# Performance work log

Hardware: AMD Instinct MI355X
Metric: run time of the kernel (lower is better)

The kernel has to match this reference:

```python
import jax, jax.numpy as jnp
import numpy as np

B, S, D, H = 1, 2048, 1024, 16
HD = D // H
FF = 4 * D
EPS_LN = 1e-5
EPS_ATTN = 1e-6


def _layernorm(x, g, b):
    mu = jnp.mean(x, axis=-1, keepdims=True)
    var = jnp.mean(jnp.square(x - mu), axis=-1, keepdims=True)
    return (x - mu) * jax.lax.rsqrt(var + EPS_LN) * g + b


def setup_inputs() -> dict:
    key = jax.random.key(0)
    ks = jax.random.split(key, 12)
    w = lambda k, shape: (jax.random.normal(k, shape, jnp.float32) * 0.02)
    return {
        "x": jax.random.normal(ks[0], (B, S, D), jnp.float32),
        "Wq": w(ks[1], (D, D)), "bq": jnp.zeros((D,), jnp.float32),
        "Wk": w(ks[2], (D, D)), "bk": jnp.zeros((D,), jnp.float32),
        "Wv": w(ks[3], (D, D)), "bv": jnp.zeros((D,), jnp.float32),
        "Wo": w(ks[4], (D, D)), "bo": jnp.zeros((D,), jnp.float32),
        "W1": w(ks[5], (FF, D)), "bb1": jnp.zeros((FF,), jnp.float32),
        "W2": w(ks[6], (D, FF)), "bb2": jnp.zeros((D,), jnp.float32),
        "g1": jnp.ones((D,), jnp.float32), "be1": jnp.zeros((D,), jnp.float32),
        "g2": jnp.ones((D,), jnp.float32), "be2": jnp.zeros((D,), jnp.float32),
    }


def reference(x, Wq, bq, Wk, bk, Wv, bv, Wo, bo, W1, bb1, W2, bb2, g1, be1, g2, be2):
    # --- pre-norm causal linear attention ---
    h = _layernorm(x, g1, be1)                     # (B,S,D)
    def heads(t):
        return t.reshape(B, S, H, HD).transpose(0, 2, 1, 3)  # (B,H,S,hd)
    q = heads(h @ Wq.T + bq)
    k = heads(h @ Wk.T + bk)
    v = heads(h @ Wv.T + bv)
    # feature map phi(x) = elu(x) + 1 (strictly positive)
    q = jax.nn.elu(q) + 1.0
    k = jax.nn.elu(k) + 1.0
    # causal cumulative state: S_t = sum_{i<=t} k_i v_i^T ; z_t = sum_{i<=t} k_i
    kv = jnp.cumsum(jnp.einsum("bhsd,bhse->bhsde", k, v), axis=2)  # (B,H,S,hd,hd)
    z = jnp.cumsum(k, axis=2)                                       # (B,H,S,hd)
    num = jnp.einsum("bhsd,bhsde->bhse", q, kv)                    # (B,H,S,hd)
    den = jnp.einsum("bhsd,bhsd->bhs", q, z) + EPS_ATTN
    attn = (num / den[..., None]).transpose(0, 2, 1, 3).reshape(B, S, D)
    attn = attn @ Wo.T + bo
    x = x + attn
    # --- FFN (GELU exact, matching torch nn.GELU default) ---
    h2 = _layernorm(x, g2, be2)
    ff = jax.nn.gelu(h2 @ W1.T + bb1, approximate=False) @ W2.T + bb2
    return x + ff
```

## Files before the change

### kernel.cpp

```cpp
#include <hip/hip_runtime.h>
#include <hip/hip_bf16.h>
#include <math.h>

constexpr int S  = 2048;
constexpr int D  = 1024;
constexpr int H  = 16;
constexpr int HD = 64;
constexpr int FF = 4096;
constexpr int NC  = 32;
constexpr int CHK = 64;
constexpr int QS  = 3 * D;

typedef __attribute__((ext_vector_type(8))) short bf16x8;
typedef __attribute__((ext_vector_type(4))) float f32x4;

__device__ inline unsigned short f2bf(float f) {
    unsigned int u = __float_as_uint(f);
    u = (u + 0x7FFFu + ((u >> 16) & 1u)) >> 16;
    return (unsigned short)u;
}

constexpr int DD4 = D * D / 4;
constexpr int FD4 = FF * D / 4;
constexpr int CVT_TOTAL4 = 4 * DD4 + 2 * FD4;
constexpr int NB_CVT  = CVT_TOTAL4 / 256;

__global__ __launch_bounds__(256) void prep(const float* __restrict__ Wq,
                                            const float* __restrict__ Wk,
                                            const float* __restrict__ Wv,
                                            const float* __restrict__ Wo,
                                            const float* __restrict__ W1,
                                            const float* __restrict__ W2,
                                            unsigned short* __restrict__ Wqkvb,
                                            unsigned short* __restrict__ Wob,
                                            unsigned short* __restrict__ W1b,
                                            unsigned short* __restrict__ W2b,
                                            const float* __restrict__ x,
                                            const float* __restrict__ g1,
                                            const float* __restrict__ be1,
                                            unsigned short* __restrict__ h1) {
    const int b = blockIdx.x, tid = threadIdx.x;
    if (b < NB_CVT) {
        int i = b * 256 + tid;
        const float* s;
        unsigned short* dp;
        if (i < DD4)                 { s = Wq + (size_t)i * 4;               dp = Wqkvb + (size_t)i * 4; }
        else if (i < 2 * DD4)        { s = Wk + (size_t)(i - DD4) * 4;       dp = Wqkvb + (size_t)i * 4; }
        else if (i < 3 * DD4)        { s = Wv + (size_t)(i - 2 * DD4) * 4;   dp = Wqkvb + (size_t)i * 4; }
        else if (i < 4 * DD4)        { s = Wo + (size_t)(i - 3 * DD4) * 4;   dp = Wob + (size_t)(i - 3 * DD4) * 4; }
        else if (i < 4 * DD4 + FD4)  { s = W1 + (size_t)(i - 4 * DD4) * 4;   dp = W1b + (size_t)(i - 4 * DD4) * 4; }
        else                         { s = W2 + (size_t)(i - 4 * DD4 - FD4) * 4; dp = W2b + (size_t)(i - 4 * DD4 - FD4) * 4; }
        float4 v = *(const float4*)s;
        ushort4 o = { f2bf(v.x), f2bf(v.y), f2bf(v.z), f2bf(v.w) };
        *(ushort4*)dp = o;
    } else {
        const int row = b - NB_CVT;
        float4 v = ((const float4*)(x + (size_t)row * D))[tid];
        float s  = v.x + v.y + v.z + v.w;
        float ss = v.x*v.x + v.y*v.y + v.z*v.z + v.w*v.w;
        #pragma unroll
        for (int off = 32; off > 0; off >>= 1) {
            s  += __shfl_down(s, off);
            ss += __shfl_down(ss, off);
        }
        __shared__ float sw[4], ssw[4];
        if ((tid & 63) == 0) { sw[tid >> 6] = s; ssw[tid >> 6] = ss; }
        __syncthreads();
        s  = sw[0] + sw[1] + sw[2] + sw[3];
        ss = ssw[0] + ssw[1] + ssw[2] + ssw[3];
        const float mu = s * (1.0f / D);
        const float rs = rsqrtf(ss * (1.0f / D) - mu * mu + 1e-5f);
        float4 gv = ((const float4*)g1)[tid];
        float4 bv = ((const float4*)be1)[tid];
        ushort4 o = { f2bf((v.x - mu) * rs * gv.x + bv.x),
                      f2bf((v.y - mu) * rs * gv.y + bv.y),
                      f2bf((v.z - mu) * rs * gv.z + bv.z),
                      f2bf((v.w - mu) * rs * gv.w + bv.w) };
        ((ushort4*)(h1 + (size_t)row * D))[tid] = o;
    }
}

template <int KS>
__global__ __launch_bounds__(256) void reduce_ln(const float* __restrict__ part,
                                                 const float* __restrict__ bias,
                                                 const float* __restrict__ res,
                                                 float* __restrict__ x2,
                                                 const float* __restrict__ g,
                                                 const float* __restrict__ b,
                                                 unsigned short* __restrict__ out) {
    const int row = blockIdx.x, tid = threadIdx.x;
    const size_t i4 = (size_t)row * 256 + tid;
    float4 a = ((const float4*)part)[i4];
    #pragma unroll
    for (int z = 1; z < KS; ++z) {
        float4 p = ((const float4*)part)[(size_t)z * S * 256 + i4];
        a.x += p.x; a.y += p.y; a.z += p.z; a.w += p.w;
    }
    float4 bi = ((const float4*)bias)[tid];
    float4 r  = ((const float4*)res)[i4];
    a.x += bi.x + r.x; a.y += bi.y + r.y; a.z += bi.z + r.z; a.w += bi.w + r.w;
    ((float4*)x2)[i4] = a;
    float s  = a.x + a.y + a.z + a.w;
    float ss = a.x*a.x + a.y*a.y + a.z*a.z + a.w*a.w;
    #pragma unroll
    for (int off = 32; off > 0; off >>= 1) {
        s  += __shfl_down(s, off);
        ss += __shfl_down(ss, off);
    }
    __shared__ float sw[4], ssw[4];
    if ((tid & 63) == 0) { sw[tid >> 6] = s; ssw[tid >> 6] = ss; }
    __syncthreads();
    s  = sw[0] + sw[1] + sw[2] + sw[3];
    ss = ssw[0] + ssw[1] + ssw[2] + ssw[3];
    const float mu = s * (1.0f / D);
    const float rs = rsqrtf(ss * (1.0f / D) - mu * mu + 1e-5f);
    float4 gv = ((const float4*)g)[tid];
    float4 bv = ((const float4*)b)[tid];
    ushort4 o = { f2bf((a.x - mu) * rs * gv.x + bv.x),
                  f2bf((a.y - mu) * rs * gv.y + bv.y),
                  f2bf((a.z - mu) * rs * gv.z + bv.z),
                  f2bf((a.w - mu) * rs * gv.w + bv.w) };
    ((ushort4*)(out + (size_t)row * D))[tid] = o;
}

template <int KS>
__global__ __launch_bounds__(256) void reduce_bias_res(const float* __restrict__ part,
                                                       const float* __restrict__ bias,
                                                       const float* __restrict__ res,
                                                       float* __restrict__ out,
                                                       int N4, int total4) {
    int i = blockIdx.x * 256 + threadIdx.x;
    if (i >= total4) return;
    float4 a = ((const float4*)part)[i];
    #pragma unroll
    for (int z = 1; z < KS; ++z) {
        float4 p = ((const float4*)part)[(size_t)z * total4 + i];
        a.x += p.x; a.y += p.y; a.z += p.z; a.w += p.w;
    }
    float4 b = ((const float4*)bias)[i % N4];
    float4 r = ((const float4*)res)[i];
    a.x += b.x + r.x; a.y += b.y + r.y; a.z += b.z + r.z; a.w += b.w + r.w;
    ((float4*)out)[i] = a;
}

enum { EPI_F32 = 0, EPI_QKV = 1, EPI_GELU_BF16 = 2, EPI_PART = 3 };

template <int EPI>
__global__ __launch_bounds__(256, 3) void gemm_bt(const unsigned short* __restrict__ A,
                                                  const unsigned short* __restrict__ W,
                                                  const float* __restrict__ bias,
                                                  const float* __restrict__ bias2,
                                                  const float* __restrict__ bias3,
                                                  void* __restrict__ outp,
                                                  int M, int N, int K, int kSplit) {
    __shared__ unsigned short As[2][64 * 64];
    __shared__ unsigned short Bs[2][128 * 64];
    const int tid  = threadIdx.x;
    const int tileM = blockIdx.x * 64;
    const int tileN = blockIdx.y * 128;
    const int w    = tid >> 6, lane = tid & 63;
    const int wm   = (w >> 1) * 32, wn = (w & 1) * 64;
    const int lr   = lane & 15, lk = lane >> 4;
    const int sw   = (lr >> 1) & 7;
    const int kLen   = K / kSplit;
    const int kStart = blockIdx.z * kLen;
    const int kEnd   = kStart + kLen;

    f32x4 acc[2][4];
    #pragma unroll
    for (int i = 0; i < 2; ++i)
        #pragma unroll
        for (int j = 0; j < 4; ++j) acc[i][j] = (f32x4)(0.0f);

    auto stage = [&](int buf, int k0) {
        #pragma unroll
        for (int p = 0; p < 2; ++p) {
            const int c   = p * 256 + tid;
            const int row = c >> 3;
            const int kc  = (c & 7) ^ ((row >> 1) & 7);
            __builtin_amdgcn_global_load_lds(
                (const __attribute__((address_space(1))) unsigned int*)
                    (A + (size_t)(tileM + row) * K + k0 + kc * 8),
                (__attribute__((address_space(3))) unsigned int*)&As[buf][c * 8],
                16, 0, 0);
        }
        #pragma unroll
        for (int p = 0; p < 4; ++p) {
            const int c   = p * 256 + tid;
            const int row = c >> 3;
            const int kc  = (c & 7) ^ ((row >> 1) & 7);
            __builtin_amdgcn_global_load_lds(
                (const __attribute__((address_space(1))) unsigned int*)
                    (W + (size_t)(tileN + row) * K + k0 + kc * 8),
                (__attribute__((address_space(3))) unsigned int*)&Bs[buf][c * 8],
                16, 0, 0);
        }
    };

    stage(0, kStart);
    __syncthreads();
    int buf = 0;
    for (int k0 = kStart; k0 < kEnd; k0 += 64) {
        if (k0 + 64 < kEnd) stage(buf ^ 1, k0 + 64);
        #pragma unroll
        for (int kk = 0; kk < 2; ++kk) {
            bf16x8 af[2], bfv[4];
            #pragma unroll
            for (int i = 0; i < 2; ++i) {
                const int row = wm + i * 16 + lr;
                af[i] = *(const bf16x8*)&As[buf][row * 64 + ((((kk << 2) | lk) ^ sw) << 3)];
            }
            #pragma unroll
            for (int j = 0; j < 4; ++j) {
                const int row = wn + j * 16 + lr;
                bfv[j] = *(const bf16x8*)&Bs[buf][row * 64 + ((((kk << 2) | lk) ^ sw) << 3)];
            }
            #pragma unroll
            for (int i = 0; i < 2; ++i)
                #pragma unroll
                for (int j = 0; j < 4; ++j)
                    acc[i][j] = __builtin_amdgcn_mfma_f32_16x16x32_bf16(af[i], bfv[j], acc[i][j], 0, 0, 0);
        }
        __syncthreads();
        buf ^= 1;
    }

    #pragma unroll
    for (int i = 0; i < 2; ++i) {
        const int rbase = tileM + wm + i * 16 + lk * 4;
        #pragma unroll
        for (int j = 0; j < 4; ++j) {
            const int col = tileN + wn + j * 16 + lr;
            #pragma unroll
            for (int r = 0; r < 4; ++r) {
                const int row = rbase + r;
                const size_t off = (size_t)row * N + col;
                float v = acc[i][j][r];
                if constexpr (EPI == EPI_PART) {
                    ((float*)outp)[(size_t)blockIdx.z * (size_t)M * (size_t)N + off] = v;
                } else if constexpr (EPI == EPI_QKV) {
                    float bc = (col < D) ? bias[col] : ((col < 2 * D) ? bias2[col - D] : bias3[col - 2 * D]);
                    v += bc;
                    if (col < 2 * D) v = v > 0.0f ? v + 1.0f : __expf(v);
                    ((float*)outp)[off] = v;
                } else if constexpr (EPI == EPI_GELU_BF16) {
                    v += bias[col];
                    float gl = 0.5f * v * (1.0f + erff(v * 0.70710678118654752f));
                    ((unsigned short*)outp)[off] = f2bf(gl);
                } else {
                    v += bias[col];
                    ((float*)outp)[off] = v;
                }
            }
        }
    }
}

__global__ __launch_bounds__(256) void attn_chunk_sums(const float* __restrict__ qkv,
                                                       float* __restrict__ KVc,
                                                       float* __restrict__ Zc) {
    const int c = blockIdx.x, h = blockIdx.y, tid = threadIdx.x;
    __shared__ float Kc[CHK * HD], Vc[CHK * HD];
    const int s0 = c * CHK;
    #pragma unroll
    for (int p = 0; p < 4; ++p) {
        int cc = p * 256 + tid;
        int t = cc >> 4, dp = (cc & 15) * 4;
        *(float4*)&Kc[t * HD + dp] = *(const float4*)(qkv + (size_t)(s0 + t) * QS + D     + h * HD + dp);
        *(float4*)&Vc[t * HD + dp] = *(const float4*)(qkv + (size_t)(s0 + t) * QS + 2 * D + h * HD + dp);
    }
    __syncthreads();
    const int d = tid >> 2, e0 = (tid & 3) * 16;
    float acc[16];
    #pragma unroll
    for (int j = 0; j < 16; ++j) acc[j] = 0.0f;
    float zacc = 0.0f;
    for (int t = 0; t < CHK; ++t) {
        float kv = Kc[t * HD + d];
        zacc += kv;
        #pragma unroll
        for (int j = 0; j < 16; ++j) acc[j] += kv * Vc[t * HD + e0 + j];
    }
    float* op = KVc + ((size_t)(h * NC + c) * HD + d) * HD + e0;
    #pragma unroll
    for (int j = 0; j < 16; ++j) op[j] = acc[j];
    if ((tid & 3) == 0) Zc[(size_t)(h * NC + c) * HD + d] = zacc;
}

__global__ __launch_bounds__(256) void attn_prefix(float* __restrict__ KVc,
                                                   float* __restrict__ Zc) {
    const int h = blockIdx.y;
    const int elem = blockIdx.x * 256 + threadIdx.x;
    size_t base = (size_t)h * NC * (HD * HD) + elem;
    float run = 0.0f;
    for (int c = 0; c < NC; ++c) {
        float t = KVc[base + (size_t)c * (HD * HD)];
        KVc[base + (size_t)c * (HD * HD)] = run;
        run += t;
    }
    if (blockIdx.x == 0 && threadIdx.x < HD) {
        size_t zb = (size_t)h * NC * HD + threadIdx.x;
        float zr = 0.0f;
        for (int c = 0; c < NC; ++c) {
            float t = Zc[zb + (size_t)c * HD];
            Zc[zb + (size_t)c * HD] = zr;
            zr += t;
        }
    }
}

__global__ __launch_bounds__(256) void attn_out(const float* __restrict__ qkv,
                                                const float* __restrict__ KVpre,
                                                const float* __restrict__ Zpre,
                                                unsigned short* __restrict__ attn) {
    const int c = blockIdx.x, h = blockIdx.y, tid = threadIdx.x;
    __shared__ float Qc[CHK * HD], KVs[CHK * HD], Pre[HD * HD], Sc[CHK * CHK];
    __shared__ float zp[HD], den[CHK];
    const int s0 = c * CHK;
    #pragma unroll
    for (int p = 0; p < 4; ++p) {
        int cc = p * 256 + tid;
        int t = cc >> 4, dp = (cc & 15) * 4;
        *(float4*)&Qc[t * HD + dp]  = *(const float4*)(qkv + (size_t)(s0 + t) * QS +     h * HD + dp);
        *(float4*)&KVs[t * HD + dp] = *(const float4*)(qkv + (size_t)(s0 + t) * QS + D + h * HD + dp);
        ((float4*)Pre)[cc] = *(const float4*)(KVpre + (size_t)(h * NC + c) * (HD * HD) + cc * 4);
    }
    if (tid < HD) zp[tid] = Zpre[(size_t)(h * NC + c) * HD + tid];
    __syncthreads();

    const int tt = tid >> 2, i0 = (tid & 3) * 16;
    for (int i = i0; i < i0 + 16; ++i) {
        float sv = 0.0f;
        for (int d2 = 0; d2 < HD; ++d2) sv += Qc[tt * HD + d2] * KVs[i * HD + d2];
        Sc[tt * CHK + i] = (i <= tt) ? sv : 0.0f;
    }
    __syncthreads();

    if (tid < CHK) {
        float dv = 1e-6f;
        for (int d2 = 0; d2 < HD; ++d2) dv += Qc[tid * HD + d2] * zp[d2];
        for (int i = 0; i < CHK; ++i) dv += Sc[tid * CHK + i];
        den[tid] = dv;
    }
    #pragma unroll
    for (int p = 0; p < 4; ++p) {
        int cc = p * 256 + tid;
        int t = cc >> 4, dp = (cc & 15) * 4;
        *(float4*)&KVs[t * HD + dp] = *(const float4*)(qkv + (size_t)(s0 + t) * QS + 2 * D + h * HD + dp);
    }
    __syncthreads();

    float o[16];
    #pragma unroll
    for (int j = 0; j < 16; ++j) o[j] = 0.0f;
    for (int d2 = 0; d2 < HD; ++d2) {
        float qv = Qc[tt * HD + d2];
        float sv = Sc[tt * CHK + d2];
        #pragma unroll
        for (int j = 0; j < 16; ++j)
            o[j] += qv * Pre[d2 * HD + i0 + j] + sv * KVs[d2 * HD + i0 + j];
    }
    const float inv = 1.0f / den[tt];
    unsigned short* op = attn + (size_t)(s0 + tt) * D + h * HD + i0;
    #pragma unroll
    for (int j0 = 0; j0 < 16; j0 += 4) {
        ushort4 ov = { f2bf(o[j0] * inv), f2bf(o[j0 + 1] * inv),
                       f2bf(o[j0 + 2] * inv), f2bf(o[j0 + 3] * inv) };
        *(ushort4*)(op + j0) = ov;
    }
}

extern "C" void kernel_launch(void* const* d_in, const int* in_sizes, int n_in,
                              void* d_out, int out_size, void* d_ws, size_t ws_size,
                              hipStream_t stream) {
    const float* x   = (const float*)d_in[0];
    const float* Wq  = (const float*)d_in[1];
    const float* bq  = (const float*)d_in[2];
    const float* Wk  = (const float*)d_in[3];
    const float* bk  = (const float*)d_in[4];
    const float* Wv  = (const float*)d_in[5];
    const float* bv  = (const float*)d_in[6];
    const float* Wo  = (const float*)d_in[7];
    const float* bo  = (const float*)d_in[8];
    const float* W1  = (const float*)d_in[9];
    const float* b1  = (const float*)d_in[10];
    const float* W2  = (const float*)d_in[11];
    const float* b2  = (const float*)d_in[12];
    const float* g1  = (const float*)d_in[13];
    const float* be1 = (const float*)d_in[14];
    const float* g2  = (const float*)d_in[15];
    const float* be2 = (const float*)d_in[16];
    float* out = (float*)d_out;

    char* wsp = (char*)d_ws;
    auto alloc = [&](size_t bytes) {
        char* p = wsp;
        wsp += (bytes + 255) & ~(size_t)255;
        return p;
    };
    unsigned short* h1   = (unsigned short*)alloc((size_t)S * D * 2);
    unsigned short* attn = (unsigned short*)alloc((size_t)S * D * 2);
    unsigned short* gbuf = (unsigned short*)alloc((size_t)S * FF * 2);
    float* x2   = (float*)alloc((size_t)S * D * 4);
    unsigned short* Wqkvb = (unsigned short*)alloc((size_t)3 * D * D * 2);
    unsigned short* Wob   = (unsigned short*)alloc((size_t)D * D * 2);
    unsigned short* W1b   = (unsigned short*)alloc((size_t)FF * D * 2);
    unsigned short* W2b   = (unsigned short*)alloc((size_t)D * FF * 2);
    float* KVc  = (float*)alloc((size_t)H * NC * HD * HD * 4);
    float* Zc   = (float*)alloc((size_t)H * NC * HD * 4);
    char* uni = (char*)alloc((size_t)32 * 1024 * 1024);
    float* qkv   = (float*)uni;
    float* parts = (float*)uni;

    prep<<<NB_CVT + S, 256, 0, stream>>>(Wq, Wk, Wv, Wo, W1, W2,
                                         Wqkvb, Wob, W1b, W2b,
                                         x, g1, be1, h1);

    gemm_bt<EPI_QKV><<<dim3(S / 64, 3 * D / 128, 1), 256, 0, stream>>>(
        h1, Wqkvb, bq, bk, bv, qkv, S, 3 * D, D, 1);

    attn_chunk_sums<<<dim3(NC, H), 256, 0, stream>>>(qkv, KVc, Zc);
    attn_prefix<<<dim3(16, H), 256, 0, stream>>>(KVc, Zc);
    attn_out<<<dim3(NC, H), 256, 0, stream>>>(qkv, KVc, Zc, attn);

    gemm_bt<EPI_PART><<<dim3(S / 64, D / 128, 2), 256, 0, stream>>>(
        attn, Wob, nullptr, nullptr, nullptr, parts, S, D, D, 2);
    reduce_ln<2><<<S, 256, 0, stream>>>(parts, bo, x, x2, g2, be2, h1);

    gemm_bt<EPI_GELU_BF16><<<dim3(S / 64, FF / 128, 1), 256, 0, stream>>>(
        h1, W1b, b1, nullptr, nullptr, gbuf, S, FF, D, 1);

    gemm_bt<EPI_PART><<<dim3(S / 64, D / 128, 4), 256, 0, stream>>>(
        gbuf, W2b, nullptr, nullptr, nullptr, parts, S, D, FF, 4);
    reduce_bias_res<4><<<(S * D / 4 + 255) / 256, 256, 0, stream>>>(
        parts, b2, x2, out, D / 4, S * D / 4);
}
```

Baseline: 288.6 us.

## Replace LDS-staged GEMM with register-direct 128x128 tiles loading fragments from global

The GEMM drops its shared-memory double buffering. Each wave now loads its MFMA fragments straight from global memory into registers, with a two-stage register prefetch. The block tile grows from 64x128 to 128x128, so each wave holds a 4x4 grid of accumulators, and the Wo projection split-K goes from 2 to 4 to keep enough blocks in flight. This removes LDS traffic and barriers. In exchange there is no sharing of operands across waves, so global and L2 traffic per FLOP is higher and register pressure rises, which may lower occupancy.

```diff
diff --git a/kernel.cpp b/kernel.cpp
--- a/kernel.cpp
+++ b/kernel.cpp
@@ -153,80 +153,60 @@
                                                   const float* __restrict__ bias3,
                                                   void* __restrict__ outp,
                                                   int M, int N, int K, int kSplit) {
-    __shared__ unsigned short As[2][64 * 64];
-    __shared__ unsigned short Bs[2][128 * 64];
     const int tid  = threadIdx.x;
-    const int tileM = blockIdx.x * 64;
+    const int tileM = blockIdx.x * 128;
     const int tileN = blockIdx.y * 128;
     const int w    = tid >> 6, lane = tid & 63;
-    const int wm   = (w >> 1) * 32, wn = (w & 1) * 64;
+    const int wm   = (w >> 1) * 64, wn = (w & 1) * 64;
     const int lr   = lane & 15, lk = lane >> 4;
-    const int sw   = (lr >> 1) & 7;
     const int kLen   = K / kSplit;
     const int kStart = blockIdx.z * kLen;
     const int kEnd   = kStart + kLen;
 
-    f32x4 acc[2][4];
-    #pragma unroll
-    for (int i = 0; i < 2; ++i)
+    const unsigned short* pA = A + (size_t)(tileM + wm + lr) * K + lk * 8;
+    const unsigned short* pB = W + (size_t)(tileN + wn + lr) * K + lk * 8;
+    const size_t rsA = (size_t)16 * K;
+
+    f32x4 acc[4][4];
+    #pragma unroll
+    for (int i = 0; i < 4; ++i)
         #pragma unroll
         for (int j = 0; j < 4; ++j) acc[i][j] = (f32x4)(0.0f);
 
-    auto stage = [&](int buf, int k0) {
-        #pragma unroll
-        for (int p = 0; p < 2; ++p) {
-            const int c   = p * 256 + tid;
-            const int row = c >> 3;
-            const int kc  = (c & 7) ^ ((row >> 1) & 7);
-            __builtin_amdgcn_global_load_lds(
-                (const __attribute__((address_space(1))) unsigned int*)
-                    (A + (size_t)(tileM + row) * K + k0 + kc * 8),
-                (__attribute__((address_space(3))) unsigned int*)&As[buf][c * 8],
-                16, 0, 0);
+    bf16x8 a0[4], b0[4], a1[4], b1[4];
+    #pragma unroll
+    for (int i = 0; i < 4; ++i) {
+        a0[i] = *(const bf16x8*)(pA + i * rsA + kStart);
+        b0[i] = *(const bf16x8*)(pB + i * rsA + kStart);
+    }
+
+    for (int k0 = kStart; k0 < kEnd; k0 += 64) {
+        #pragma unroll
+        for (int i = 0; i < 4; ++i) {
+            a1[i] = *(const bf16x8*)(pA + i * rsA + k0 + 32);
+            b1[i] = *(const bf16x8*)(pB + i * rsA + k0 + 32);
         }
         #pragma unroll
-        for (int p = 0; p < 4; ++p) {
-            const int c   = p * 256 + tid;
-            const int row = c >> 3;
-            const int kc  = (c & 7) ^ ((row >> 1) & 7);
-            __builtin_amdgcn_global_load_lds(
-                (const __attribute__((address_space(1))) unsigned int*)
-                    (W + (size_t)(tileN + row) * K + k0 + kc * 8),
-                (__attribute__((address_space(3))) unsigned int*)&Bs[buf][c * 8],
-                16, 0, 0);
+        for (int i = 0; i < 4; ++i)
+            #pragma unroll
+            for (int j = 0; j < 4; ++j)
+                acc[i][j] = __builtin_amdgcn_mfma_f32_16x16x32_bf16(a0[i], b0[j], acc[i][j], 0, 0, 0);
+        if (k0 + 64 < kEnd) {
+            #pragma unroll
+            for (int i = 0; i < 4; ++i) {
+                a0[i] = *(const bf16x8*)(pA + i * rsA + k0 + 64);
+                b0[i] = *(const bf16x8*)(pB + i * rsA + k0 + 64);
+            }
         }
-    };
-
-    stage(0, kStart);
-    __syncthreads();
-    int buf = 0;
-    for (int k0 = kStart; k0 < kEnd; k0 += 64) {
-        if (k0 + 64 < kEnd) stage(buf ^ 1, k0 + 64);
-        #pragma unroll
-        for (int kk = 0; kk < 2; ++kk) {
-            bf16x8 af[2], bfv[4];
+        #pragma unroll
+        for (int i = 0; i < 4; ++i)
             #pragma unroll
-            for (int i = 0; i < 2; ++i) {
-                const int row = wm + i * 16 + lr;
-                af[i] = *(const bf16x8*)&As[buf][row * 64 + ((((kk << 2) | lk) ^ sw) << 3)];
-            }
-            #pragma unroll
-            for (int j = 0; j < 4; ++j) {
-                const int row = wn + j * 16 + lr;
-                bfv[j] = *(const bf16x8*)&Bs[buf][row * 64 + ((((kk << 2) | lk) ^ sw) << 3)];
-            }
-            #pragma unroll
-            for (int i = 0; i < 2; ++i)
-                #pragma unroll
-                for (int j = 0; j < 4; ++j)
-                    acc[i][j] = __builtin_amdgcn_mfma_f32_16x16x32_bf16(af[i], bfv[j], acc[i][j], 0, 0, 0);
-        }
-        __syncthreads();
-        buf ^= 1;
-    }
-
-    #pragma unroll
-    for (int i = 0; i < 2; ++i) {
+            for (int j = 0; j < 4; ++j)
+                acc[i][j] = __builtin_amdgcn_mfma_f32_16x16x32_bf16(a1[i], b1[j], acc[i][j], 0, 0, 0);
+    }
+
+    #pragma unroll
+    for (int i = 0; i < 4; ++i) {
         const int rbase = tileM + wm + i * 16 + lk * 4;
         #pragma unroll
         for (int j = 0; j < 4; ++j) {
@@ -416,21 +396,21 @@
                                          Wqkvb, Wob, W1b, W2b,
                                          x, g1, be1, h1);
 
-    gemm_bt<EPI_QKV><<<dim3(S / 64, 3 * D / 128, 1), 256, 0, stream>>>(
+    gemm_bt<EPI_QKV><<<dim3(S / 128, 3 * D / 128, 1), 256, 0, stream>>>(
         h1, Wqkvb, bq, bk, bv, qkv, S, 3 * D, D, 1);
 
     attn_chunk_sums<<<dim3(NC, H), 256, 0, stream>>>(qkv, KVc, Zc);
     attn_prefix<<<dim3(16, H), 256, 0, stream>>>(KVc, Zc);
     attn_out<<<dim3(NC, H), 256, 0, stream>>>(qkv, KVc, Zc, attn);
 
-    gemm_bt<EPI_PART><<<dim3(S / 64, D / 128, 2), 256, 0, stream>>>(
-        attn, Wob, nullptr, nullptr, nullptr, parts, S, D, D, 2);
-    reduce_ln<2><<<S, 256, 0, stream>>>(parts, bo, x, x2, g2, be2, h1);
-
-    gemm_bt<EPI_GELU_BF16><<<dim3(S / 64, FF / 128, 1), 256, 0, stream>>>(
+    gemm_bt<EPI_PART><<<dim3(S / 128, D / 128, 4), 256, 0, stream>>>(
+        attn, Wob, nullptr, nullptr, nullptr, parts, S, D, D, 4);
+    reduce_ln<4><<<S, 256, 0, stream>>>(parts, bo, x, x2, g2, be2, h1);
+
+    gemm_bt<EPI_GELU_BF16><<<dim3(S / 128, FF / 128, 1), 256, 0, stream>>>(
         h1, W1b, b1, nullptr, nullptr, gbuf, S, FF, D, 1);
 
-    gemm_bt<EPI_PART><<<dim3(S / 64, D / 128, 4), 256, 0, stream>>>(
+    gemm_bt<EPI_PART><<<dim3(S / 128, D / 128, 4), 256, 0, stream>>>(
         gbuf, W2b, nullptr, nullptr, nullptr, parts, S, D, FF, 4);
     reduce_bias_res<4><<<(S * D / 4 + 255) / 256, 256, 0, stream>>>(
         parts, b2, x2, out, D / 4, S * D / 4);
```

Result: slower. 406.5 us (+40.8%).
